# Optimization experiments

Measured on AMD Instinct MI355X. Metric: run time of the kernel, lower is better.

## Reference

```python
import jax, jax.numpy as jnp
import numpy as np

B, T, A = 4096, 32, 3
HID, D, N, K = 1024, 128, 16, 4096
FLAT = T * A            # 96
LAT = N * D             # 2048
COMMIT = 0.25


def setup_inputs() -> dict:
    key = jax.random.key(0)
    ks = jax.random.split(key, 14)
    s = 0.02
    return {
        "actions": jax.random.normal(ks[0], (B, T, A), jnp.float32),
        # encoder: FLAT -> HID -> HID -> N*D
        "e_w1": jax.random.normal(ks[1], (FLAT, HID), jnp.float32) * s,
        "e_b1": jnp.zeros((HID,), jnp.float32),
        "e_w2": jax.random.normal(ks[2], (HID, HID), jnp.float32) * s,
        "e_b2": jnp.zeros((HID,), jnp.float32),
        "e_w3": jax.random.normal(ks[3], (HID, LAT), jnp.float32) * s,
        "e_b3": jnp.zeros((LAT,), jnp.float32),
        # codebook init: uniform(-1/K, 1/K) as in torch init
        "codebook": jax.random.uniform(ks[4], (K, D), jnp.float32, -1.0 / K, 1.0 / K),
        # decoder: N*D -> HID -> HID -> FLAT
        "d_w1": jax.random.normal(ks[5], (LAT, HID), jnp.float32) * s,
        "d_b1": jnp.zeros((HID,), jnp.float32),
        "d_w2": jax.random.normal(ks[6], (HID, HID), jnp.float32) * s,
        "d_b2": jnp.zeros((HID,), jnp.float32),
        "d_w3": jax.random.normal(ks[7], (HID, FLAT), jnp.float32) * s,
        "d_b3": jnp.zeros((FLAT,), jnp.float32),
    }


def reference(actions, e_w1, e_b1, e_w2, e_b2, e_w3, e_b3, codebook,
              d_w1, d_b1, d_w2, d_b2, d_w3, d_b3):
    sg = jax.lax.stop_gradient
    b = actions.shape[0]
    # encode: [B, T*A] -> [B, N, D]
    flat = actions.reshape(b, FLAT)
    h = jax.nn.silu(flat @ e_w1 + e_b1)
    h = jax.nn.silu(h @ e_w2 + e_b2)
    latents = (h @ e_w3 + e_b3).reshape(b, N, D)
    # nearest-code search: [B*N, K] squared distances
    fl = latents.reshape(b * N, D)
    dist = (fl * fl).sum(1, keepdims=True) + (codebook * codebook).sum(1)[None, :] - 2.0 * (fl @ codebook.T)
    indices = jnp.argmin(dist, axis=1).reshape(b, N)
    quantized = codebook[indices]                      # [B, N, D]
    codebook_loss = jnp.mean((quantized - sg(latents)) ** 2)
    commitment_loss = jnp.mean((latents - sg(quantized)) ** 2)
    vq_loss = codebook_loss + COMMIT * commitment_loss
    q_st = latents + sg(quantized - latents)           # straight-through
    # decode
    g = jax.nn.silu(q_st.reshape(b, LAT) @ d_w1 + d_b1)
    g = jax.nn.silu(g @ d_w2 + d_b2)
    recon = (g @ d_w3 + d_b3).reshape(b, T, A)
    recon_loss = jnp.mean((recon - actions) ** 2)
    loss = recon_loss + vq_loss
    return recon, indices, vq_loss, recon_loss, loss
```

## Files before the change

### kernel.cpp

```cpp
#include <hip/hip_runtime.h>
#include <hip/hip_bf16.h>

#define DD 128

typedef float f2v __attribute__((ext_vector_type(2)));

__global__ void plant_diag(float val, float* out) {
    if (threadIdx.x == 0 && blockIdx.x == 0) out[0] = val;
}

__global__ void zero_acc(double* acc) {
    if (threadIdx.x == 0 && blockIdx.x == 0) { acc[0] = 0.0; acc[1] = 0.0; }
}

__device__ __forceinline__ float silu_np(float x) {
    float e = (float)exp(-(double)x);
    float u = 1.0f + e;
    float v = 1.0f / u;
    return x * v;
}

__global__ void w_pack(const float* __restrict__ W, float* __restrict__ Wp,
                       int K, int N, int K32, int total) {
    int gid = blockIdx.x * 256 + threadIdx.x;
    if (gid >= total) return;
    int c = gid & 63;
    int k = (gid >> 6) % K32;
    int pn = gid / (K32 * 64);
    int n = pn * 64 + c;
    Wp[gid] = (k < K && n < N) ? W[(size_t)k * N + n] : 0.0f;
}

template <bool SILU>
__global__ __launch_bounds__(256) void gemm_wp(const float* __restrict__ A,
                                               const float* __restrict__ Wp,
                                               const float* __restrict__ bias,
                                               float* __restrict__ C,
                                               int M, int N, int K) {
    __shared__ __align__(16) float As[128][36];
    const int t = threadIdx.x;
    const int tx = t & 15, ty = t >> 4;
    const int bm = blockIdx.y * 128, bn = blockIdx.x * 64;
    const int K32 = ((K + 31) / 32) * 32;

    float acc[8][4];
#pragma unroll
    for (int i = 0; i < 8; ++i)
#pragma unroll
        for (int j = 0; j < 4; ++j) acc[i][j] = 0.0f;

    const int nPanels = (K + 31) / 32;
    float ra[16];

    {
        const int k0 = 0;
#pragma unroll
        for (int it = 0; it < 16; ++it) {
            int e = t + 256 * it;
            int m = e >> 5, kk = e & 31;
            int mm = bm + m; if (mm >= M) mm = M - 1;
            int kc = k0 + kk;
            ra[it] = (kc < K) ? A[(size_t)mm * K + kc] : 0.0f;
        }
    }

    const float* wpc = Wp + (size_t)blockIdx.x * K32 * 64 + 4 * tx + 1024;

    for (int p = 0; p < nPanels; ++p) {
        __syncthreads();
#pragma unroll
        for (int it = 0; it < 16; ++it) {
            int e = t + 256 * it;
            As[e >> 5][e & 31] = ra[it];
        }
        __syncthreads();

        if (p + 1 < nPanels) {
            const int k0 = (p + 1) * 32;
#pragma unroll
            for (int it = 0; it < 16; ++it) {
                int e = t + 256 * it;
                int m = e >> 5, kk = e & 31;
                int mm = bm + m; if (mm >= M) mm = M - 1;
                int kc = k0 + kk;
                ra[it] = (kc < K) ? A[(size_t)mm * K + kc] : 0.0f;
            }
        }

        const float* wq = wpc + (size_t)p * 2048;
#pragma unroll
        for (int kq = 0; kq < 8; ++kq) {
            float4 a4[8], w4[4];
#pragma unroll
            for (int i = 0; i < 8; ++i)
                a4[i] = *(const float4*)&As[ty + 16 * i][4 * kq];
#pragma unroll
            for (int q = 0; q < 4; ++q)
                w4[q] = *(const float4*)(wq + (4 * kq + q) * 64 - 1024);
#pragma unroll
            for (int q = 0; q < 4; ++q) {
                const float wv[4] = {w4[q].x, w4[q].y, w4[q].z, w4[q].w};
#pragma unroll
                for (int i = 0; i < 8; ++i) {
                    const float av = ((const float*)&a4[i])[q];
#pragma unroll
                    for (int j = 0; j < 4; ++j)
                        acc[i][j] = fmaf(av, wv[j], acc[i][j]);
                }
            }
        }
    }

#pragma unroll
    for (int i = 0; i < 8; ++i) {
        int m = bm + ty + 16 * i;
#pragma unroll
        for (int j = 0; j < 4; ++j) {
            int n = bn + 4 * tx + j;
            if (m < M && n < N) {
                float x = acc[i][j] + bias[n];
                if (SILU) x = silu_np(x);
                C[(size_t)m * N + n] = x;
            }
        }
    }
}

template <bool SILU>
__global__ __launch_bounds__(256) void gemm_db(const float* __restrict__ A,
                                               const float* __restrict__ W,
                                               const float* __restrict__ bias,
                                               float* __restrict__ C,
                                               int M, int N, int K) {
    __shared__ __align__(16) float As[128][36];
    __shared__ __align__(16) float Ws[32][68];
    const int t = threadIdx.x;
    const int tx = t & 15, ty = t >> 4;
    const int bm = blockIdx.y * 128, bn = blockIdx.x * 64;

    float acc[8][4];
#pragma unroll
    for (int i = 0; i < 8; ++i)
#pragma unroll
        for (int j = 0; j < 4; ++j) acc[i][j] = 0.0f;

    const int nPanels = (K + 31) / 32;
    float ra[16], rw[8];

    {
        const int k0 = 0;
#pragma unroll
        for (int it = 0; it < 16; ++it) {
            int e = t + 256 * it;
            int m = e >> 5, kk = e & 31;
            int mm = bm + m; if (mm >= M) mm = M - 1;
            int kc = k0 + kk;
            ra[it] = (kc < K) ? A[(size_t)mm * K + kc] : 0.0f;
        }
#pragma unroll
        for (int it = 0; it < 8; ++it) {
            int e = t + 256 * it;
            int r = e >> 6, c = e & 63;
            int n = bn + c;
            int kr = k0 + r;
            rw[it] = (kr < K && n < N) ? W[(size_t)kr * N + n] : 0.0f;
        }
    }

    for (int p = 0; p < nPanels; ++p) {
        __syncthreads();
#pragma unroll
        for (int it = 0; it < 16; ++it) {
            int e = t + 256 * it;
            As[e >> 5][e & 31] = ra[it];
        }
#pragma unroll
        for (int it = 0; it < 8; ++it) {
            int e = t + 256 * it;
            Ws[e >> 6][e & 63] = rw[it];
        }
        __syncthreads();

        if (p + 1 < nPanels) {
            const int k0 = (p + 1) * 32;
#pragma unroll
            for (int it = 0; it < 16; ++it) {
                int e = t + 256 * it;
                int m = e >> 5, kk = e & 31;
                int mm = bm + m; if (mm >= M) mm = M - 1;
                int kc = k0 + kk;
                ra[it] = (kc < K) ? A[(size_t)mm * K + kc] : 0.0f;
            }
#pragma unroll
            for (int it = 0; it < 8; ++it) {
                int e = t + 256 * it;
                int r = e >> 6, c = e & 63;
                int n = bn + c;
                int kr = k0 + r;
                rw[it] = (kr < K && n < N) ? W[(size_t)kr * N + n] : 0.0f;
            }
        }

#pragma unroll
        for (int kq = 0; kq < 8; ++kq) {
            float4 a4[8], w4[4];
#pragma unroll
            for (int i = 0; i < 8; ++i)
                a4[i] = *(const float4*)&As[ty + 16 * i][4 * kq];
#pragma unroll
            for (int q = 0; q < 4; ++q)
                w4[q] = *(const float4*)&Ws[4 * kq + q][4 * tx];
#pragma unroll
            for (int q = 0; q < 4; ++q) {
                const float wv[4] = {w4[q].x, w4[q].y, w4[q].z, w4[q].w};
#pragma unroll
                for (int i = 0; i < 8; ++i) {
                    const float av = ((const float*)&a4[i])[q];
#pragma unroll
                    for (int j = 0; j < 4; ++j)
                        acc[i][j] = fmaf(av, wv[j], acc[i][j]);
                }
            }
        }
    }

#pragma unroll
    for (int i = 0; i < 8; ++i) {
        int m = bm + ty + 16 * i;
#pragma unroll
        for (int j = 0; j < 4; ++j) {
            int n = bn + 4 * tx + j;
            if (m < M && n < N) {
                float x = acc[i][j] + bias[n];
                if (SILU) x = silu_np(x);
                C[(size_t)m * N + n] = x;
            }
        }
    }
}

__device__ __forceinline__ float pairwise128_sq(const float* __restrict__ x, int stride) {
    float r0 = x[0*stride]*x[0*stride], r1 = x[1*stride]*x[1*stride],
          r2 = x[2*stride]*x[2*stride], r3 = x[3*stride]*x[3*stride],
          r4 = x[4*stride]*x[4*stride], r5 = x[5*stride]*x[5*stride],
          r6 = x[6*stride]*x[6*stride], r7 = x[7*stride]*x[7*stride];
    for (int i = 8; i < 128; i += 8) {
        r0 += x[(i+0)*stride]*x[(i+0)*stride];
        r1 += x[(i+1)*stride]*x[(i+1)*stride];
        r2 += x[(i+2)*stride]*x[(i+2)*stride];
        r3 += x[(i+3)*stride]*x[(i+3)*stride];
        r4 += x[(i+4)*stride]*x[(i+4)*stride];
        r5 += x[(i+5)*stride]*x[(i+5)*stride];
        r6 += x[(i+6)*stride]*x[(i+6)*stride];
        r7 += x[(i+7)*stride]*x[(i+7)*stride];
    }
    return ((r0 + r1) + (r2 + r3)) + ((r4 + r5) + (r6 + r7));
}

__global__ void code_t2(const float* __restrict__ cb, float* __restrict__ t2, int K) {
    int k = blockIdx.x * 256 + threadIdx.x;
    if (k >= K) return;
    t2[k] = pairwise128_sq(cb + (size_t)k * DD, 1);
}

__global__ void cb_pack(const float* __restrict__ cb, float* __restrict__ cbP, int total) {
    int gid = blockIdx.x * 256 + threadIdx.x;
    if (gid >= total) return;
    int pair = gid >> 8;
    int r = gid & 255;
    int d = r >> 1, w = r & 1;
    cbP[gid] = cb[(size_t)(2 * pair + w) * DD + d];
}

#define VQG_ROWS 128
#define VQG_CPP  256
#define VQG_LT   132

__global__ __launch_bounds__(512) void vq_g88p(const float* __restrict__ lat,
                                               const float* __restrict__ cbP,
                                               const float* __restrict__ t2,
                                               float* __restrict__ pbv,
                                               int* __restrict__ pbk,
                                               int K, int rows_total) {
    __shared__ __align__(16) float Ls[VQG_ROWS][VQG_LT];
    __shared__ float T1s[VQG_ROWS];
    __shared__ float bwv[8][VQG_ROWS];
    __shared__ int   bwk[8][VQG_ROWS];

    const int t = threadIdx.x;
    const int tx = t & 15, ty = t >> 4;
    const int wave = t >> 6, lane = t & 63;
    const int r0 = blockIdx.x * VQG_ROWS;

#pragma unroll
    for (int it = 0; it < 8; ++it) {
        int g = t + 512 * it;
        int r = g >> 5, dq = g & 31;
        int rr = r0 + r; if (rr >= rows_total) rr = rows_total - 1;
        const float4 lv = *(const float4*)(lat + (size_t)rr * DD + 4 * dq);
        *(float4*)&Ls[r][4 * dq] = lv;
    }
    __syncthreads();

    if (t < VQG_ROWS) {
        const float* xr = &Ls[t][0];
        float4 q0 = *(const float4*)&xr[0];
        float4 q1 = *(const float4*)&xr[4];
        float a0 = q0.x*q0.x, a1 = q0.y*q0.y, a2 = q0.z*q0.z, a3 = q0.w*q0.w;
        float a4 = q1.x*q1.x, a5 = q1.y*q1.y, a6 = q1.z*q1.z, a7 = q1.w*q1.w;
#pragma unroll
        for (int i = 1; i < 16; ++i) {
            q0 = *(const float4*)&xr[8 * i];
            q1 = *(const float4*)&xr[8 * i + 4];
            a0 += q0.x*q0.x; a1 += q0.y*q0.y; a2 += q0.z*q0.z; a3 += q0.w*q0.w;
            a4 += q1.x*q1.x; a5 += q1.y*q1.y; a6 += q1.z*q1.z; a7 += q1.w*q1.w;
        }
        T1s[t] = ((a0 + a1) + (a2 + a3)) + ((a4 + a5) + (a6 + a7));
    }
    __syncthreads();

    float t1r[8];
#pragma unroll
    for (int i = 0; i < 8; ++i) t1r[i] = T1s[tx + 16 * i];

    float bestv[8]; int bestk[8];
#pragma unroll
    for (int i = 0; i < 8; ++i) { bestv[i] = 3.4e38f; bestk[i] = 0; }

    const int NP = K / VQG_CPP;
#pragma unroll 1
    for (int p = 0; p < NP; ++p) {
        const int kp = p * VQG_CPP;
        const int cbase = kp + 8 * ty;
        const float* cp0 = cbP + (size_t)cbase * DD;
        float t2v[8];
#pragma unroll
        for (int j = 0; j < 8; ++j) t2v[j] = t2[cbase + j];

        f2v s2[8][4];
#pragma unroll
        for (int i = 0; i < 8; ++i)
#pragma unroll
            for (int m = 0; m < 4; ++m) s2[i][m] = (f2v)(0.0f);

#pragma unroll 4
        for (int dq = 0; dq < 32; ++dq) {
            float4 u0[4], u1[4];
#pragma unroll
            for (int m = 0; m < 4; ++m) {
                u0[m] = *(const float4*)(cp0 + m * 256 + 8 * dq);
                u1[m] = *(const float4*)(cp0 + m * 256 + 8 * dq + 4);
            }
#pragma unroll
            for (int i = 0; i < 8; ++i) {
                const float4 la = *(const float4*)&Ls[tx + 16 * i][4 * dq];
                const f2v lx = {la.x, la.x}, ly = {la.y, la.y};
                const f2v lz = {la.z, la.z}, lw = {la.w, la.w};
#pragma unroll
                for (int m = 0; m < 4; ++m) {
                    const f2v c0 = {u0[m].x, u0[m].y};
                    const f2v c1 = {u0[m].z, u0[m].w};
                    const f2v c2 = {u1[m].x, u1[m].y};
                    const f2v c3 = {u1[m].z, u1[m].w};
                    s2[i][m] = __builtin_elementwise_fma(lx, c0, s2[i][m]);
                    s2[i][m] = __builtin_elementwise_fma(ly, c1, s2[i][m]);
                    s2[i][m] = __builtin_elementwise_fma(lz, c2, s2[i][m]);
                    s2[i][m] = __builtin_elementwise_fma(lw, c3, s2[i][m]);
                }
            }
        }

#pragma unroll
        for (int i = 0; i < 8; ++i) {
            const float tt1 = t1r[i];
#pragma unroll
            for (int m = 0; m < 4; ++m) {
                const int c0 = cbase + 2 * m;
                const float d0 = (tt1 + t2v[2 * m + 0]) - 2.0f * s2[i][m].x;
                const float d1 = (tt1 + t2v[2 * m + 1]) - 2.0f * s2[i][m].y;
                if (d0 < bestv[i]) { bestv[i] = d0; bestk[i] = c0; }
                if (d1 < bestv[i]) { bestv[i] = d1; bestk[i] = c0 + 1; }
            }
        }
    }

#pragma unroll
    for (int off = 16; off <= 32; off <<= 1) {
#pragma unroll
        for (int i = 0; i < 8; ++i) {
            float vv = __shfl_xor(bestv[i], off);
            int kk = __shfl_xor(bestk[i], off);
            if (vv < bestv[i] || (vv == bestv[i] && kk < bestk[i])) {
                bestv[i] = vv; bestk[i] = kk;
            }
        }
    }
    if (lane < 16) {
#pragma unroll
        for (int i = 0; i < 8; ++i) {
            bwv[wave][tx + 16 * i] = bestv[i];
            bwk[wave][tx + 16 * i] = bestk[i];
        }
    }
    __syncthreads();
    if (t < VQG_ROWS) {
        float bv = bwv[0][t]; int bk = bwk[0][t];
#pragma unroll
        for (int w = 1; w < 8; ++w) {
            float v = bwv[w][t]; int k = bwk[w][t];
            if (v < bv || (v == bv && k < bk)) { bv = v; bk = k; }
        }
        if (r0 + t < rows_total) {
            pbv[r0 + t] = bv;
            pbk[r0 + t] = bk;
        }
    }
}

__global__ __launch_bounds__(512) void vq_np4(const float* __restrict__ lat,
                                              const float* __restrict__ cb,
                                              const float* __restrict__ t2,
                                              float* __restrict__ pbv,
                                              int* __restrict__ pbk,
                                              int K, int Kc, int rows_total) {
    __shared__ __align__(16) float Ls[128][68];
    __shared__ __align__(16) float Cs[128][68];
    __shared__ float T1s[64];
    __shared__ float T2s[64];
    __shared__ float bwv[8][68];
    __shared__ int   bwk[8][68];

    const int t = threadIdx.x;
    const int tx = t & 15, ty = t >> 4;
    const int wave = t >> 6, lane = t & 63;
    const int r0 = blockIdx.x * 64;
    const int kbeg = blockIdx.y * Kc;
    const int kend = kbeg + Kc;

#pragma unroll
    for (int it = 0; it < 4; ++it) {
        int g = t + 512 * it;
        int row = g >> 5, dq = g & 31;
        int rr = r0 + row; if (rr >= rows_total) rr = rows_total - 1;
        const float4 v = *(const float4*)(lat + (size_t)rr * DD + 4 * dq);
        Ls[4*dq+0][row] = v.x; Ls[4*dq+1][row] = v.y;
        Ls[4*dq+2][row] = v.z; Ls[4*dq+3][row] = v.w;
    }
    __syncthreads();
    if (t < 64) T1s[t] = pairwise128_sq(&Ls[0][t], 68);

    float bestv[4]; int bestk[4];
#pragma unroll
    for (int r = 0; r < 4; ++r) { bestv[r] = 3.4e38f; bestk[r] = 0; }

    float4 pc[4];
    float pt2 = 0.0f;
#pragma unroll
    for (int it = 0; it < 4; ++it) {
        int g = t + 512 * it;
        int c = g >> 5, dq = g & 31;
        int cc = kbeg + c; if (cc >= K) cc = K - 1;
        pc[it] = *(const float4*)(cb + (size_t)cc * DD + 4 * dq);
    }
    if (t < 64) { int cc = kbeg + t; if (cc >= K) cc = K - 1; pt2 = t2[cc]; }

    for (int k0 = kbeg; k0 < kend; k0 += 64) {
        __syncthreads();
#pragma unroll
        for (int it = 0; it < 4; ++it) {
            int g = t + 512 * it;
            int c = g >> 5, dq = g & 31;
            Cs[4*dq+0][c] = pc[it].x; Cs[4*dq+1][c] = pc[it].y;
            Cs[4*dq+2][c] = pc[it].z; Cs[4*dq+3][c] = pc[it].w;
        }
        if (t < 64) T2s[t] = pt2;
        __syncthreads();

        if (k0 + 64 < kend) {
            const int kn = k0 + 64;
#pragma unroll
            for (int it = 0; it < 4; ++it) {
                int g = t + 512 * it;
                int c = g >> 5, dq = g & 31;
                int cc = kn + c; if (cc >= K) cc = K - 1;
                pc[it] = *(const float4*)(cb + (size_t)cc * DD + 4 * dq);
            }
            if (t < 64) { int cc = kn + t; if (cc >= K) cc = K - 1; pt2 = t2[cc]; }
        }

        float s[4][2];
#pragma unroll
        for (int r = 0; r < 4; ++r) { s[r][0] = 0.0f; s[r][1] = 0.0f; }

#pragma unroll 8
        for (int d = 0; d < 128; ++d) {
            const float4 a4 = *(const float4*)&Ls[d][4 * tx];
            const float2 c2 = *(const float2*)&Cs[d][2 * ty];
            const float av[4] = {a4.x, a4.y, a4.z, a4.w};
#pragma unroll
            for (int r = 0; r < 4; ++r) {
                s[r][0] = fmaf(av[r], c2.x, s[r][0]);
                s[r][1] = fmaf(av[r], c2.y, s[r][1]);
            }
        }

#pragma unroll
        for (int r = 0; r < 4; ++r) {
            const float t1 = T1s[4 * tx + r];
#pragma unroll
            for (int j = 0; j < 2; ++j) {
                int kc = k0 + 2 * ty + j;
                float dist = (t1 + T2s[2 * ty + j]) - 2.0f * s[r][j];
                if (kc < K && dist < bestv[r]) { bestv[r] = dist; bestk[r] = kc; }
            }
        }
    }

#pragma unroll
    for (int off = 16; off <= 32; off <<= 1) {
#pragma unroll
        for (int r = 0; r < 4; ++r) {
            float vv = __shfl_xor(bestv[r], off);
            int kk = __shfl_xor(bestk[r], off);
            if (vv < bestv[r] || (vv == bestv[r] && kk < bestk[r])) {
                bestv[r] = vv; bestk[r] = kk;
            }
        }
    }
    if (lane < 16) {
#pragma unroll
        for (int r = 0; r < 4; ++r) {
            bwv[wave][4 * lane + r] = bestv[r];
            bwk[wave][4 * lane + r] = bestk[r];
        }
    }
    __syncthreads();
    if (t < 64) {
        float bv = bwv[0][t]; int bk = bwk[0][t];
#pragma unroll
        for (int w = 1; w < 8; ++w) {
            float v = bwv[w][t]; int k = bwk[w][t];
            if (v < bv || (v == bv && k < bk)) { bv = v; bk = k; }
        }
        if (r0 + t < rows_total) {
            size_t o = (size_t)blockIdx.y * rows_total + (r0 + t);
            pbv[o] = bv;
            pbk[o] = bk;
        }
    }
}

__global__ __launch_bounds__(256) void vq_combine(const float* __restrict__ pbv,
                                                  const int* __restrict__ pbk,
                                                  int S, int rows,
                                                  int* __restrict__ indices,
                                                  double* __restrict__ acc) {
    int r = blockIdx.x * 256 + threadIdx.x;
    float bv = 3.4e38f; int bk = 0;
    if (r < rows) {
        for (int s = 0; s < S; ++s) {
            float v = pbv[(size_t)s * rows + r];
            int k = pbk[(size_t)s * rows + r];
            if (v < bv) { bv = v; bk = k; }
        }
        indices[r] = bk;
    }
    __shared__ double red[256];
    red[threadIdx.x] = (r < rows) ? (double)bv : 0.0;
    __syncthreads();
    for (int s = 128; s > 0; s >>= 1) {
        if (threadIdx.x < s) red[threadIdx.x] += red[threadIdx.x + s];
        __syncthreads();
    }
    if (threadIdx.x == 0) atomicAdd(acc, red[0]);
}

__global__ void q_gather(const int* __restrict__ idx, const float* __restrict__ cb,
                         float* __restrict__ Q, int count, int nlat) {
    int gid = blockIdx.x * 256 + threadIdx.x;
    if (gid >= count) return;
    int m = gid >> 11;
    int j = gid & 2047;
    int code = idx[m * nlat + (j >> 7)];
    Q[gid] = cb[((size_t)code << 7) + (j & 127)];
}

__global__ __launch_bounds__(256) void recon_out(const float* __restrict__ recon,
                                                 const float* __restrict__ actions,
                                                 float* __restrict__ out,
                                                 double* __restrict__ acc, int count) {
    int gid = blockIdx.x * 256 + threadIdx.x;
    double sq = 0.0;
    if (gid < count) {
        float rv = recon[gid];
        float av = actions[gid];
        double diff = (double)rv - (double)av;
        out[gid] = rv;
        sq = diff * diff;
    }
    __shared__ double red[256];
    red[threadIdx.x] = sq;
    __syncthreads();
    for (int s = 128; s > 0; s >>= 1) {
        if (threadIdx.x < s) red[threadIdx.x] += red[threadIdx.x + s];
        __syncthreads();
    }
    if (threadIdx.x == 0) atomicAdd(acc + 1, red[0]);
}

__global__ void idx_out(const int* __restrict__ idx, float* __restrict__ out, int count) {
    int gid = blockIdx.x * 256 + threadIdx.x;
    if (gid < count) out[gid] = (float)idx[gid];
}

__global__ void finalize(const double* __restrict__ acc, float* __restrict__ out,
                         double vq_den, double rec_den) {
    double vq = 1.25 * acc[0] / vq_den;
    double rl = acc[1] / rec_den;
    out[0] = (float)vq;
    out[1] = (float)rl;
    out[2] = (float)(rl + vq);
}

static inline int ceildiv(int a, int b) { return (a + b - 1) / b; }

extern "C" void kernel_launch(void* const* d_in, const int* in_sizes, int n_in,
                              void* d_out, int out_size, void* d_ws, size_t ws_size,
                              hipStream_t stream) {
    const float* actions = (const float*)d_in[0];
    const float* e_w1 = (const float*)d_in[1];
    const float* e_b1 = (const float*)d_in[2];
    const float* e_w2 = (const float*)d_in[3];
    const float* e_b2 = (const float*)d_in[4];
    const float* e_w3 = (const float*)d_in[5];
    const float* e_b3 = (const float*)d_in[6];
    const float* cb   = (const float*)d_in[7];
    const float* d_w1 = (const float*)d_in[8];
    const float* d_b1 = (const float*)d_in[9];
    const float* d_w2 = (const float*)d_in[10];
    const float* d_b2 = (const float*)d_in[11];
    const float* d_w3 = (const float*)d_in[12];
    const float* d_b3 = (const float*)d_in[13];
    float* out = (float*)d_out;

    const int FLAT = in_sizes[13];
    const int B    = in_sizes[0] / FLAT;
    const int HID  = in_sizes[2];
    const int LAT  = in_sizes[6];
    const int K    = in_sizes[7] / DD;
    const int NL   = LAT / DD;

    const bool g88 = (K % VQG_CPP == 0);
    const int S = 1;
    const int Kc = K;

    const float* wsrc[6] = {e_w1, e_w2, e_w3, d_w1, d_w2, d_w3};
    const int wK[6] = {FLAT, HID, HID, LAT, HID, HID};
    const int wN[6] = {HID, HID, LAT, HID, HID, FLAT};
    size_t wpOff[6];
    size_t wpTot = 0;
    for (int i = 0; i < 6; ++i) {
        int K32 = ceildiv(wK[i], 32) * 32;
        int Pn = ceildiv(wN[i], 64);
        wpOff[i] = wpTot;
        wpTot += (size_t)Pn * K32 * 64;
    }

    int CHUNK = B;
    bool useWp = true;
    auto need = [&](int ch, bool wp) -> size_t {
        return (size_t)ch * HID * 4 * 2 + (size_t)ch * LAT * 4 * 2
             + (size_t)ch * HID * 4 * 2 + (size_t)ch * FLAT * 4
             + (size_t)K * 4 + (size_t)K * DD * 4 + (wp ? wpTot * 4 : 0)
             + 64 + (size_t)B * NL * 4
             + (size_t)ch * NL * S * 8;
    };
    if (need(B, true) > ws_size) useWp = false;
    while (CHUNK > 16 && need(CHUNK, useWp) > ws_size) CHUNK >>= 1;
    if (need(CHUNK, useWp) > ws_size) {
        plant_diag<<<1, 64, 0, stream>>>(2222.0f, out);
        return;
    }
    const int NCHUNK = ceildiv(B, CHUNK);

    char* ws = (char*)d_ws;
    size_t off = 0;
    float* h1c  = (float*)(ws + off); off += (size_t)CHUNK * HID * 4;
    float* h2c  = (float*)(ws + off); off += (size_t)CHUNK * HID * 4;
    float* latc = (float*)(ws + off); off += (size_t)CHUNK * LAT * 4;
    float* Qc   = (float*)(ws + off); off += (size_t)CHUNK * LAT * 4;
    float* g1c  = (float*)(ws + off); off += (size_t)CHUNK * HID * 4;
    float* g2c  = (float*)(ws + off); off += (size_t)CHUNK * HID * 4;
    float* recc = (float*)(ws + off); off += (size_t)CHUNK * FLAT * 4;
    float* t2   = (float*)(ws + off); off += (size_t)K * 4;
    float* cbP  = (float*)(ws + off); off += (size_t)K * DD * 4;
    float* Wp   = (float*)(ws + off); off += useWp ? wpTot * 4 : 0;
    double* acc = (double*)(ws + off); off += 64;
    int*   idx  = (int*)(ws + off);   off += (size_t)B * NL * 4;
    float* pbv  = (float*)(ws + off); off += (size_t)CHUNK * NL * S * 4;
    int*   pbk  = (int*)(ws + off);

    zero_acc<<<1, 64, 0, stream>>>(acc);
    code_t2<<<ceildiv(K, 256), 256, 0, stream>>>(cb, t2, K);
    if (g88) {
        cb_pack<<<ceildiv(K * DD, 256), 256, 0, stream>>>(cb, cbP, K * DD);
    }
    if (useWp) {
        for (int i = 0; i < 6; ++i) {
            int K32 = ceildiv(wK[i], 32) * 32;
            int Pn = ceildiv(wN[i], 64);
            int total = Pn * K32 * 64;
            w_pack<<<ceildiv(total, 256), 256, 0, stream>>>(
                wsrc[i], Wp + wpOff[i], wK[i], wN[i], K32, total);
        }
    }

    auto GEMM = [&](int li, bool silu, const float* Araw, const float* bias, float* Cout,
                    int M, int N, int Kd) {
        dim3 grid(ceildiv(N, 64), ceildiv(M, 128));
        if (useWp) {
            if (silu) gemm_wp<true><<<grid, 256, 0, stream>>>(Araw, Wp + wpOff[li], bias, Cout, M, N, Kd);
            else      gemm_wp<false><<<grid, 256, 0, stream>>>(Araw, Wp + wpOff[li], bias, Cout, M, N, Kd);
        } else {
            if (silu) gemm_db<true><<<grid, 256, 0, stream>>>(Araw, wsrc[li], bias, Cout, M, N, Kd);
            else      gemm_db<false><<<grid, 256, 0, stream>>>(Araw, wsrc[li], bias, Cout, M, N, Kd);
        }
    };

    for (int c = 0; c < NCHUNK; ++c) {
        const int r0 = c * CHUNK;
        const int cbR = (B - r0 < CHUNK) ? (B - r0) : CHUNK;
        const float* act_c = actions + (size_t)r0 * FLAT;
        int* idx_c = idx + (size_t)r0 * NL;
        const int rows = cbR * NL;

        GEMM(0, true,  act_c, e_b1, h1c, cbR, HID, FLAT);
        GEMM(1, true,  h1c,   e_b2, h2c, cbR, HID, HID);
        GEMM(2, false, h2c,   e_b3, latc, cbR, LAT, HID);

        if (g88) {
            vq_g88p<<<ceildiv(rows, VQG_ROWS), 512, 0, stream>>>(
                latc, cbP, t2, pbv, pbk, K, rows);
        } else {
            vq_np4<<<dim3(ceildiv(rows, 64), S), 512, 0, stream>>>(
                latc, cb, t2, pbv, pbk, K, Kc, rows);
        }
        vq_combine<<<ceildiv(rows, 256), 256, 0, stream>>>(pbv, pbk, S, rows, idx_c, acc);

        q_gather<<<ceildiv(cbR * LAT, 256), 256, 0, stream>>>(idx_c, cb, Qc, cbR * LAT, NL);
        GEMM(3, true,  Qc,  d_b1, g1c, cbR, HID, LAT);
        GEMM(4, true,  g1c, d_b2, g2c, cbR, HID, HID);
        GEMM(5, false, g2c, d_b3, recc, cbR, FLAT, HID);

        recon_out<<<ceildiv(cbR * FLAT, 256), 256, 0, stream>>>(
            recc, act_c, out + (size_t)r0 * FLAT, acc, cbR * FLAT);
    }

    idx_out<<<ceildiv(B * NL, 256), 256, 0, stream>>>(idx, out + (size_t)B * FLAT, B * NL);
    finalize<<<1, 1, 0, stream>>>(acc, out + (size_t)B * FLAT + (size_t)B * NL,
                                  (double)B * NL * DD, (double)B * FLAT);
}
```

Before: 1.907 ms.

## Drop packed-weight GEMM path, use LDS-staged weights and 64-row tiles for narrow N

Removes the per-call weight packing kernels and the gemm_wp kernel, which read weights straight from a packed global buffer. All GEMMs now use gemm_db, which stages weight tiles in shared memory. A new gemm64 kernel with 64x64 tiles handles narrow outputs (N<128, the final 96-wide decoder layer) to launch more blocks. This saves six packing launches and their extra weight traffic, but the kernel no longer benefits from coalesced packed-weight reads.

Measured after the change: 1.806 ms. 1.06x faster.

```diff
diff --git a/kernel.cpp b/kernel.cpp
--- a/kernel.cpp
+++ b/kernel.cpp
@@ -18,112 +18,6 @@
     float u = 1.0f + e;
     float v = 1.0f / u;
     return x * v;
-}
-
-__global__ void w_pack(const float* __restrict__ W, float* __restrict__ Wp,
-                       int K, int N, int K32, int total) {
-    int gid = blockIdx.x * 256 + threadIdx.x;
-    if (gid >= total) return;
-    int c = gid & 63;
-    int k = (gid >> 6) % K32;
-    int pn = gid / (K32 * 64);
-    int n = pn * 64 + c;
-    Wp[gid] = (k < K && n < N) ? W[(size_t)k * N + n] : 0.0f;
-}
-
-template <bool SILU>
-__global__ __launch_bounds__(256) void gemm_wp(const float* __restrict__ A,
-                                               const float* __restrict__ Wp,
-                                               const float* __restrict__ bias,
-                                               float* __restrict__ C,
-                                               int M, int N, int K) {
-    __shared__ __align__(16) float As[128][36];
-    const int t = threadIdx.x;
-    const int tx = t & 15, ty = t >> 4;
-    const int bm = blockIdx.y * 128, bn = blockIdx.x * 64;
-    const int K32 = ((K + 31) / 32) * 32;
-
-    float acc[8][4];
-#pragma unroll
-    for (int i = 0; i < 8; ++i)
-#pragma unroll
-        for (int j = 0; j < 4; ++j) acc[i][j] = 0.0f;
-
-    const int nPanels = (K + 31) / 32;
-    float ra[16];
-
-    {
-        const int k0 = 0;
-#pragma unroll
-        for (int it = 0; it < 16; ++it) {
-            int e = t + 256 * it;
-            int m = e >> 5, kk = e & 31;
-            int mm = bm + m; if (mm >= M) mm = M - 1;
-            int kc = k0 + kk;
-            ra[it] = (kc < K) ? A[(size_t)mm * K + kc] : 0.0f;
-        }
-    }
-
-    const float* wpc = Wp + (size_t)blockIdx.x * K32 * 64 + 4 * tx + 1024;
-
-    for (int p = 0; p < nPanels; ++p) {
-        __syncthreads();
-#pragma unroll
-        for (int it = 0; it < 16; ++it) {
-            int e = t + 256 * it;
-            As[e >> 5][e & 31] = ra[it];
-        }
-        __syncthreads();
-
-        if (p + 1 < nPanels) {
-            const int k0 = (p + 1) * 32;
-#pragma unroll
-            for (int it = 0; it < 16; ++it) {
-                int e = t + 256 * it;
-                int m = e >> 5, kk = e & 31;
-                int mm = bm + m; if (mm >= M) mm = M - 1;
-                int kc = k0 + kk;
-                ra[it] = (kc < K) ? A[(size_t)mm * K + kc] : 0.0f;
-            }
-        }
-
-        const float* wq = wpc + (size_t)p * 2048;
-#pragma unroll
-        for (int kq = 0; kq < 8; ++kq) {
-            float4 a4[8], w4[4];
-#pragma unroll
-            for (int i = 0; i < 8; ++i)
-                a4[i] = *(const float4*)&As[ty + 16 * i][4 * kq];
-#pragma unroll
-            for (int q = 0; q < 4; ++q)
-                w4[q] = *(const float4*)(wq + (4 * kq + q) * 64 - 1024);
-#pragma unroll
-            for (int q = 0; q < 4; ++q) {
-                const float wv[4] = {w4[q].x, w4[q].y, w4[q].z, w4[q].w};
-#pragma unroll
-                for (int i = 0; i < 8; ++i) {
-                    const float av = ((const float*)&a4[i])[q];
-#pragma unroll
-                    for (int j = 0; j < 4; ++j)
-                        acc[i][j] = fmaf(av, wv[j], acc[i][j]);
-                }
-            }
-        }
-    }
-
-#pragma unroll
-    for (int i = 0; i < 8; ++i) {
-        int m = bm + ty + 16 * i;
-#pragma unroll
-        for (int j = 0; j < 4; ++j) {
-            int n = bn + 4 * tx + j;
-            if (m < M && n < N) {
-                float x = acc[i][j] + bias[n];
-                if (SILU) x = silu_np(x);
-                C[(size_t)m * N + n] = x;
-            }
-        }
-    }
 }
 
 template <bool SILU>
@@ -227,6 +121,107 @@
 #pragma unroll
     for (int i = 0; i < 8; ++i) {
         int m = bm + ty + 16 * i;
+#pragma unroll
+        for (int j = 0; j < 4; ++j) {
+            int n = bn + 4 * tx + j;
+            if (m < M && n < N) {
+                float x = acc[i][j] + bias[n];
+                if (SILU) x = silu_np(x);
+                C[(size_t)m * N + n] = x;
+            }
+        }
+    }
+}
+
+template <bool SILU>
+__global__ __launch_bounds__(256) void gemm64(const float* __restrict__ A,
+                                              const float* __restrict__ W,
+                                              const float* __restrict__ bias,
+                                              float* __restrict__ C,
+                                              int M, int N, int K) {
+    __shared__ __align__(16) float As[64][36];
+    __shared__ __align__(16) float Ws[32][68];
+    const int t = threadIdx.x;
+    const int tx = t & 15, ty = t >> 4;
+    const int bm = blockIdx.y * 64, bn = blockIdx.x * 64;
+
+    float acc[4][4];
+#pragma unroll
+    for (int i = 0; i < 4; ++i)
+#pragma unroll
+        for (int j = 0; j < 4; ++j) acc[i][j] = 0.0f;
+
+    const int nPanels = (K + 31) / 32;
+    float ra[8], rw[8];
+
+    {
+        const int k0 = 0;
+#pragma unroll
+        for (int it = 0; it < 8; ++it) {
+            int e = t + 256 * it;
+            int m = e >> 5, kk = e & 31;
+            int mm = bm + m; if (mm >= M) mm = M - 1;
+            int kc = k0 + kk;
+            ra[it] = (kc < K) ? A[(size_t)mm * K + kc] : 0.0f;
+            int r = e >> 6, c = e & 63;
+            int n = bn + c;
+            int kr = k0 + r;
+            rw[it] = (kr < K && n < N) ? W[(size_t)kr * N + n] : 0.0f;
+        }
+    }
+
+    for (int p = 0; p < nPanels; ++p) {
+        __syncthreads();
+#pragma unroll
+        for (int it = 0; it < 8; ++it) {
+            int e = t + 256 * it;
+            As[e >> 5][e & 31] = ra[it];
+            Ws[e >> 6][e & 63] = rw[it];
+        }
+        __syncthreads();
+
+        if (p + 1 < nPanels) {
+            const int k0 = (p + 1) * 32;
+#pragma unroll
+            for (int it = 0; it < 8; ++it) {
+                int e = t + 256 * it;
+                int m = e >> 5, kk = e & 31;
+                int mm = bm + m; if (mm >= M) mm = M - 1;
+                int kc = k0 + kk;
+                ra[it] = (kc < K) ? A[(size_t)mm * K + kc] : 0.0f;
+                int r = e >> 6, c = e & 63;
+                int n = bn + c;
+                int kr = k0 + r;
+                rw[it] = (kr < K && n < N) ? W[(size_t)kr * N + n] : 0.0f;
+            }
+        }
+
+#pragma unroll
+        for (int kq = 0; kq < 8; ++kq) {
+            float4 a4[4], w4[4];
+#pragma unroll
+            for (int i = 0; i < 4; ++i)
+                a4[i] = *(const float4*)&As[4 * ty + i][4 * kq];
+#pragma unroll
+            for (int q = 0; q < 4; ++q)
+                w4[q] = *(const float4*)&Ws[4 * kq + q][4 * tx];
+#pragma unroll
+            for (int q = 0; q < 4; ++q) {
+                const float wv[4] = {w4[q].x, w4[q].y, w4[q].z, w4[q].w};
+                const float av[4] = {((const float*)&a4[0])[q], ((const float*)&a4[1])[q],
+                                     ((const float*)&a4[2])[q], ((const float*)&a4[3])[q]};
+#pragma unroll
+                for (int i = 0; i < 4; ++i)
+#pragma unroll
+                    for (int j = 0; j < 4; ++j)
+                        acc[i][j] = fmaf(av[i], wv[j], acc[i][j]);
+            }
+        }
+    }
+
+#pragma unroll
+    for (int i = 0; i < 4; ++i) {
+        int m = bm + 4 * ty + i;
 #pragma unroll
         for (int j = 0; j < 4; ++j) {
             int n = bn + 4 * tx + j;
@@ -654,30 +649,15 @@
     const int S = 1;
     const int Kc = K;
 
-    const float* wsrc[6] = {e_w1, e_w2, e_w3, d_w1, d_w2, d_w3};
-    const int wK[6] = {FLAT, HID, HID, LAT, HID, HID};
-    const int wN[6] = {HID, HID, LAT, HID, HID, FLAT};
-    size_t wpOff[6];
-    size_t wpTot = 0;
-    for (int i = 0; i < 6; ++i) {
-        int K32 = ceildiv(wK[i], 32) * 32;
-        int Pn = ceildiv(wN[i], 64);
-        wpOff[i] = wpTot;
-        wpTot += (size_t)Pn * K32 * 64;
-    }
-
     int CHUNK = B;
-    bool useWp = true;
-    auto need = [&](int ch, bool wp) -> size_t {
+    auto need = [&](int ch) -> size_t {
         return (size_t)ch * HID * 4 * 2 + (size_t)ch * LAT * 4 * 2
              + (size_t)ch * HID * 4 * 2 + (size_t)ch * FLAT * 4
-             + (size_t)K * 4 + (size_t)K * DD * 4 + (wp ? wpTot * 4 : 0)
-             + 64 + (size_t)B * NL * 4
+             + (size_t)K * 4 + (size_t)K * DD * 4 + 64 + (size_t)B * NL * 4
              + (size_t)ch * NL * S * 8;
     };
-    if (need(B, true) > ws_size) useWp = false;
-    while (CHUNK > 16 && need(CHUNK, useWp) > ws_size) CHUNK >>= 1;
-    if (need(CHUNK, useWp) > ws_size) {
+    while (CHUNK > 16 && need(CHUNK) > ws_size) CHUNK >>= 1;
+    if (need(CHUNK) > ws_size) {
         plant_diag<<<1, 64, 0, stream>>>(2222.0f, out);
         return;
     }
@@ -694,7 +674,6 @@
     float* recc = (float*)(ws + off); off += (size_t)CHUNK * FLAT * 4;
     float* t2   = (float*)(ws + off); off += (size_t)K * 4;
     float* cbP  = (float*)(ws + off); off += (size_t)K * DD * 4;
-    float* Wp   = (float*)(ws + off); off += useWp ? wpTot * 4 : 0;
     double* acc = (double*)(ws + off); off += 64;
     int*   idx  = (int*)(ws + off);   off += (size_t)B * NL * 4;
     float* pbv  = (float*)(ws + off); off += (size_t)CHUNK * NL * S * 4;
@@ -705,25 +684,17 @@
     if (g88) {
         cb_pack<<<ceildiv(K * DD, 256), 256, 0, stream>>>(cb, cbP, K * DD);
     }
-    if (useWp) {
-        for (int i = 0; i < 6; ++i) {
-            int K32 = ceildiv(wK[i], 32) * 32;
-            int Pn = ceildiv(wN[i], 64);
-            int total = Pn * K32 * 64;
-            w_pack<<<ceildiv(total, 256), 256, 0, stream>>>(
-                wsrc[i], Wp + wpOff[i], wK[i], wN[i], K32, total);
-        }
-    }
-
-    auto GEMM = [&](int li, bool silu, const float* Araw, const float* bias, float* Cout,
-                    int M, int N, int Kd) {
-        dim3 grid(ceildiv(N, 64), ceildiv(M, 128));
-        if (useWp) {
-            if (silu) gemm_wp<true><<<grid, 256, 0, stream>>>(Araw, Wp + wpOff[li], bias, Cout, M, N, Kd);
-            else      gemm_wp<false><<<grid, 256, 0, stream>>>(Araw, Wp + wpOff[li], bias, Cout, M, N, Kd);
+
+    auto GEMM = [&](bool silu, const float* Araw, const float* Wt, const float* bias,
+                    float* Cout, int M, int N, int Kd) {
+        if (N < 128) {
+            dim3 grid(ceildiv(N, 64), ceildiv(M, 64));
+            if (silu) gemm64<true><<<grid, 256, 0, stream>>>(Araw, Wt, bias, Cout, M, N, Kd);
+            else      gemm64<false><<<grid, 256, 0, stream>>>(Araw, Wt, bias, Cout, M, N, Kd);
         } else {
-            if (silu) gemm_db<true><<<grid, 256, 0, stream>>>(Araw, wsrc[li], bias, Cout, M, N, Kd);
-            else      gemm_db<false><<<grid, 256, 0, stream>>>(Araw, wsrc[li], bias, Cout, M, N, Kd);
+            dim3 grid(ceildiv(N, 64), ceildiv(M, 128));
+            if (silu) gemm_db<true><<<grid, 256, 0, stream>>>(Araw, Wt, bias, Cout, M, N, Kd);
+            else      gemm_db<false><<<grid, 256, 0, stream>>>(Araw, Wt, bias, Cout, M, N, Kd);
         }
     };
 
@@ -734,9 +705,9 @@
         int* idx_c = idx + (size_t)r0 * NL;
         const int rows = cbR * NL;
 
-        GEMM(0, true,  act_c, e_b1, h1c, cbR, HID, FLAT);
-        GEMM(1, true,  h1c,   e_b2, h2c, cbR, HID, HID);
-        GEMM(2, false, h2c,   e_b3, latc, cbR, LAT, HID);
+        GEMM(true,  act_c, e_w1, e_b1, h1c, cbR, HID, FLAT);
+        GEMM(true,  h1c,   e_w2, e_b2, h2c, cbR, HID, HID);
+        GEMM(false, h2c,   e_w3, e_b3, latc, cbR, LAT, HID);
 
         if (g88) {
             vq_g88p<<<ceildiv(rows, VQG_ROWS), 512, 0, stream>>>(
@@ -748,9 +719,9 @@
         vq_combine<<<ceildiv(rows, 256), 256, 0, stream>>>(pbv, pbk, S, rows, idx_c, acc);
 
         q_gather<<<ceildiv(cbR * LAT, 256), 256, 0, stream>>>(idx_c, cb, Qc, cbR * LAT, NL);
-        GEMM(3, true,  Qc,  d_b1, g1c, cbR, HID, LAT);
-        GEMM(4, true,  g1c, d_b2, g2c, cbR, HID, HID);
-        GEMM(5, false, g2c, d_b3, recc, cbR, FLAT, HID);
+        GEMM(true,  Qc,  d_w1, d_b1, g1c, cbR, HID, LAT);
+        GEMM(true,  g1c, d_w2, d_b2, g2c, cbR, HID, HID);
+        GEMM(false, g2c, d_w3, d_b3, recc, cbR, FLAT, HID);
 
         recon_out<<<ceildiv(cbR * FLAT, 256), 256, 0, stream>>>(
             recc, act_c, out + (size_t)r0 * FLAT, acc, cbR * FLAT);
```
